# Performance work log

Hardware: AMD Instinct MI355X
Metric: run time of the kernel (lower is better)

## Reference

```python
import jax, jax.numpy as jnp
import numpy as np

EMBED_DIM = 1024
NUM_HEADS = 16
HEAD_DIM = EMBED_DIM // NUM_HEADS
SCALE = HEAD_DIM ** -0.5


def setup_inputs() -> dict:
    key = jax.random.key(0)
    ks = jax.random.split(key, 9)
    B, S, D = 32, 577, EMBED_DIM
    std = 1.0 / np.sqrt(D)
    inp = {
        "hidden_states": jax.random.normal(ks[0], (B, S, D), dtype=jnp.float32),
        "q_w": jax.random.normal(ks[1], (D, D), dtype=jnp.float32) * std,
        "q_b": jax.random.normal(ks[2], (D,), dtype=jnp.float32) * 0.01,
        "k_w": jax.random.normal(ks[3], (D, D), dtype=jnp.float32) * std,
        "k_b": jax.random.normal(ks[4], (D,), dtype=jnp.float32) * 0.01,
        "v_w": jax.random.normal(ks[5], (D, D), dtype=jnp.float32) * std,
        "v_b": jax.random.normal(ks[6], (D,), dtype=jnp.float32) * 0.01,
        "o_w": jax.random.normal(ks[7], (D, D), dtype=jnp.float32) * std,
        "o_b": jax.random.normal(ks[8], (D,), dtype=jnp.float32) * 0.01,
    }
    return inp


def reference(hidden_states, q_w, q_b, k_w, k_b, v_w, v_b, o_w, o_b):
    B, S, D = hidden_states.shape
    H, Dh = NUM_HEADS, HEAD_DIM

    def proj(w, b):
        # torch Linear: x @ w.T + b ; reshape to [B, H, S, Dh]
        y = jnp.einsum('bsd,ed->bse', hidden_states, w) + b
        return y.reshape(B, S, H, Dh).transpose(0, 2, 1, 3)

    q = proj(q_w, q_b)
    k = proj(k_w, k_b)
    v = proj(v_w, v_b)

    scores = jnp.einsum('bhqd,bhkd->bhqk', q * SCALE, k)  # [B,H,S,S]
    attn = jax.nn.softmax(scores, axis=-1)
    out = jnp.einsum('bhqk,bhkd->bhqd', attn, v)  # [B,H,S,Dh]
    out = out.transpose(0, 2, 1, 3).reshape(B, S, D)
    return jnp.einsum('bsd,ed->bse', out, o_w) + o_b
```

## Files before the change

### kernel.cpp

```cpp
#include <hip/hip_runtime.h>
#include <hip/hip_bf16.h>
#include <stdint.h>

#define B_   32
#define S_   577
#define SP   640
#define D_   1024
#define H_   16
#define DH   64
#define BH_  (B_*H_)
#define M_   (B_*S_)
#define MP2  18688
#define SCALE_ 0.125f
#define LOG2E_ 1.44269504088896f

typedef __bf16 bf16;
typedef __bf16 bf16x8 __attribute__((ext_vector_type(8)));
typedef __bf16 bf16x4 __attribute__((ext_vector_type(4)));
typedef float  f32x4  __attribute__((ext_vector_type(4)));

__device__ __forceinline__ void gload16(const bf16* g, bf16* l) {
    __builtin_amdgcn_global_load_lds((__attribute__((address_space(1))) void*)g,
                                     (__attribute__((address_space(3))) void*)l, 16, 0, 0);
}

__global__ void cast_kernel(const float* __restrict__ in, bf16* __restrict__ out, int n4) {
    int i = blockIdx.x * blockDim.x + threadIdx.x;
    if (i >= n4) return;
    float4 v = ((const float4*)in)[i];
    bf16x4 o;
    o[0] = (bf16)v.x; o[1] = (bf16)v.y; o[2] = (bf16)v.z; o[3] = (bf16)v.w;
    ((bf16x4*)out)[i] = o;
}

__global__ void cast4_kernel(const float* __restrict__ w0, const float* __restrict__ w1,
                             const float* __restrict__ w2, const float* __restrict__ w3,
                             bf16* __restrict__ o0, bf16* __restrict__ o1,
                             bf16* __restrict__ o2, bf16* __restrict__ o3) {
    int i = blockIdx.x * blockDim.x + threadIdx.x;
    int seg = i >> 18, r = i & 262143;
    const float* in = (seg == 0) ? w0 : (seg == 1) ? w1 : (seg == 2) ? w2 : w3;
    bf16* out       = (seg == 0) ? o0 : (seg == 1) ? o1 : (seg == 2) ? o2 : o3;
    float4 v = ((const float4*)in)[r];
    bf16x4 o;
    o[0] = (bf16)v.x; o[1] = (bf16)v.y; o[2] = (bf16)v.z; o[3] = (bf16)v.w;
    ((bf16x4*)out)[r] = o;
}

__device__ __forceinline__ void stage256(const bf16* __restrict__ A, const bf16* __restrict__ B,
                                         int m0, int n0, int K, int kt, bf16* SMbuf) {
    const int tid = threadIdx.x;
    const int wave = tid >> 6;
    #pragma unroll
    for (int ld = 0; ld < 8; ++ld) {
        int li  = ld * 512 + tid;
        int row = (li >> 3) & 255;
        int ch  = (li & 7) ^ (row & 7);
        const bf16* g = ((ld < 4) ? (A + (size_t)(m0 + row) * K)
                                  : (B + (size_t)(n0 + row) * K)) + kt * 64 + ch * 8;
        bf16* l = SMbuf + (size_t)(ld * 512 + wave * 64) * 8;
        gload16(g, l);
    }
}

__device__ __forceinline__ void compute256(const bf16* SMbuf, f32x4 acc[8][4],
                                           int wm, int wn, int r16, int c4) {
    #pragma unroll
    for (int kk = 0; kk < 2; ++kk) {
        bf16x8 bq[4];
        #pragma unroll
        for (int j = 0; j < 4; ++j) {
            int row = wn * 64 + j * 16 + r16;
            int c   = (kk * 4 + c4) ^ (row & 7);
            bq[j] = *(const bf16x8*)(SMbuf + 16384 + row * 64 + c * 8);
        }
        #pragma unroll
        for (int i = 0; i < 8; ++i) {
            int row = wm * 128 + i * 16 + r16;
            int c   = (kk * 4 + c4) ^ (row & 7);
            bf16x8 a = *(const bf16x8*)(SMbuf + row * 64 + c * 8);
            #pragma unroll
            for (int j = 0; j < 4; ++j)
                acc[i][j] = __builtin_amdgcn_mfma_f32_16x16x32_bf16(a, bq[j], acc[i][j], 0, 0, 0);
        }
    }
}

__global__ __launch_bounds__(512, 2) void gemm_qkv(const bf16* __restrict__ A, const bf16* __restrict__ Bw,
                                                   const float* __restrict__ qb, const float* __restrict__ kb,
                                                   const float* __restrict__ vb,
                                                   bf16* __restrict__ qk, bf16* __restrict__ vT) {
    __shared__ __align__(16) bf16 SM[2 * 32768];
    const int bx = blockIdx.x;
    const int bm = bx / 12, bn = bx % 12;
    const int m0 = bm * 256, n0 = bn * 256;
    const int tid = threadIdx.x;
    const int lane = tid & 63, wave = tid >> 6;
    const int wm = wave >> 2, wn = wave & 3;
    const int r16 = lane & 15, c4 = lane >> 4;

    f32x4 acc[8][4];
    #pragma unroll
    for (int i = 0; i < 8; ++i)
        #pragma unroll
        for (int j = 0; j < 4; ++j)
            #pragma unroll
            for (int r = 0; r < 4; ++r) acc[i][j][r] = 0.0f;

    stage256(A, Bw, m0, n0, 1024, 0, SM);
    __syncthreads();
    for (int kt = 0; kt < 16; ++kt) {
        if (kt < 15) stage256(A, Bw, m0, n0, 1024, kt + 1, SM + ((kt + 1) & 1) * 32768);
        compute256(SM + (kt & 1) * 32768, acc, wm, wn, r16, c4);
        __syncthreads();
    }

    if (bn < 8) {
        const float* barr = (bn < 4) ? qb : kb;
        const float mul = (bn < 4) ? SCALE_ * LOG2E_ : 1.0f;
        #pragma unroll
        for (int j = 0; j < 4; ++j) {
            int n = n0 + wn * 64 + j * 16 + r16;
            float bias = barr[n & 1023];
            #pragma unroll
            for (int i = 0; i < 8; ++i) {
                #pragma unroll
                for (int r = 0; r < 4; ++r) {
                    int m = m0 + wm * 128 + i * 16 + c4 * 4 + r;
                    if (m < M_) qk[(size_t)m * 2048 + n] = (bf16)((acc[i][j][r] + bias) * mul);
                }
            }
        }
    } else {
        const int bnp = bn - 8;
        bf16* Ts = SM;
        #pragma unroll
        for (int mh = 0; mh < 2; ++mh) {
            if (wm == mh) {
                #pragma unroll
                for (int j = 0; j < 4; ++j) {
                    int nl = wn * 64 + j * 16 + r16;
                    float bias = vb[bnp * 256 + nl];
                    #pragma unroll
                    for (int i = 0; i < 8; ++i) {
                        #pragma unroll
                        for (int r = 0; r < 4; ++r) {
                            int tr = i * 16 + c4 * 4 + r;
                            Ts[tr * 259 + nl] = (bf16)(acc[i][j][r] + bias);
                        }
                    }
                }
            }
            __syncthreads();
            {
                int ml = tid & 127, nh = tid >> 7;
                int gm = m0 + mh * 128 + ml;
                if (gm < M_) {
                    unsigned bb = (unsigned)gm / 577u, s = (unsigned)gm - bb * 577u;
                    bf16* dst = vT + ((size_t)((bb * 16 + bnp * 4 + nh) * 64)) * SP + s;
                    const bf16* src = Ts + ml * 259 + nh * 64;
                    #pragma unroll 8
                    for (int j = 0; j < 64; ++j) dst[(size_t)j * SP] = src[j];
                }
            }
            __syncthreads();
        }
    }
}

__global__ __launch_bounds__(512, 2) void gemm_out(const bf16* __restrict__ A, const bf16* __restrict__ Bw,
                                                   const float* __restrict__ ob, float* __restrict__ out) {
    __shared__ __align__(16) bf16 SM[2 * 32768];
    const int bx = blockIdx.x;
    const int bm = bx >> 2, bn = bx & 3;
    const int m0 = bm * 256, n0 = bn * 256;
    const int tid = threadIdx.x;
    const int lane = tid & 63, wave = tid >> 6;
    const int wm = wave >> 2, wn = wave & 3;
    const int r16 = lane & 15, c4 = lane >> 4;

    f32x4 acc[8][4];
    #pragma unroll
    for (int i = 0; i < 8; ++i)
        #pragma unroll
        for (int j = 0; j < 4; ++j)
            #pragma unroll
            for (int r = 0; r < 4; ++r) acc[i][j][r] = 0.0f;

    stage256(A, Bw, m0, n0, 1024, 0, SM);
    __syncthreads();
    for (int kt = 0; kt < 16; ++kt) {
        if (kt < 15) stage256(A, Bw, m0, n0, 1024, kt + 1, SM + ((kt + 1) & 1) * 32768);
        compute256(SM + (kt & 1) * 32768, acc, wm, wn, r16, c4);
        __syncthreads();
    }

    #pragma unroll
    for (int j = 0; j < 4; ++j) {
        int n = n0 + wn * 64 + j * 16 + r16;
        float bias = ob[n];
        #pragma unroll
        for (int i = 0; i < 8; ++i) {
            #pragma unroll
            for (int r = 0; r < 4; ++r) {
                int m = m0 + wm * 128 + i * 16 + c4 * 4 + r;
                if (m < M_) out[(size_t)m * 1024 + n] = acc[i][j][r] + bias;
            }
        }
    }
}

__global__ __launch_bounds__(256) void attn_kernel(const bf16* __restrict__ qk,
                                                   const bf16* __restrict__ vT, bf16* __restrict__ obuf) {
    __shared__ __align__(16) bf16 KV[2][2][4096];
    __shared__ __align__(16) char Pls[4 * 2 * 2048];
    const int orig = blockIdx.x;
    const int xcd = orig & 7;
    const int t   = orig >> 3;
    const int qt  = t % 5, bhg = t / 5;
    const int bh  = bhg * 8 + xcd;
    const int b   = bh >> 4, h = bh & 15;
    const int tid = threadIdx.x;
    const int lane = tid & 63, wave = tid >> 6;
    const int r16 = lane & 15, c4 = lane >> 4;
    const int q0  = qt * 128 + wave * 32;
    const int swz = (r16 & 7) << 4;

    const bf16* qp = qk + (size_t)(b * 577) * 2048 + h * 64;
    const bf16* kp = qp + 1024;
    const bf16* vp = vT + (size_t)bh * 64 * SP;

    bf16x8 aq[2][2];
    #pragma unroll
    for (int qf = 0; qf < 2; ++qf)
        #pragma unroll
        for (int c = 0; c < 2; ++c)
            aq[qf][c] = *(const bf16x8*)(qp + (size_t)(q0 + qf * 16 + r16) * 2048 + c * 32 + c4 * 8);

    float mi[2] = {-3.0e38f, -3.0e38f};
    float li[2] = {0.0f, 0.0f};
    f32x4 accO[2][4];
    #pragma unroll
    for (int qf = 0; qf < 2; ++qf)
        #pragma unroll
        for (int nt = 0; nt < 4; ++nt)
            #pragma unroll
            for (int r = 0; r < 4; ++r) accO[qf][nt][r] = 0.0f;

    char* pbase = Pls + wave * 4096 + r16 * 128;

    auto stageKV = [&](int kt, int buf) {
        #pragma unroll
        for (int half = 0; half < 2; ++half) {
            int li  = half * 256 + tid;
            int row = li >> 3;
            int ch  = (li & 7) ^ (row & 7);
            bf16* lk = &KV[buf][0][(size_t)(half * 256 + wave * 64) * 8];
            bf16* lv = &KV[buf][1][(size_t)(half * 256 + wave * 64) * 8];
            gload16(kp + (size_t)(kt * 64 + row) * 2048 + ch * 8, lk);
            gload16(vp + (size_t)row * SP + kt * 64 + ch * 8, lv);
        }
    };

    stageKV(0, 0);
    __syncthreads();

    for (int kt = 0; kt < 10; ++kt) {
        const int buf = kt & 1;
        if (kt < 9) stageKV(kt + 1, buf ^ 1);

        bf16x8 kf[4][2];
        #pragma unroll
        for (int nt = 0; nt < 4; ++nt)
            #pragma unroll
            for (int c = 0; c < 2; ++c) {
                int row = nt * 16 + r16;
                int cc  = (c * 4 + c4) ^ (row & 7);
                kf[nt][c] = *(const bf16x8*)(&KV[buf][0][row * 64 + cc * 8]);
            }
        f32x4 sc[2][4];
        #pragma unroll
        for (int qf = 0; qf < 2; ++qf)
            #pragma unroll
            for (int nt = 0; nt < 4; ++nt) {
                f32x4 z = {0.0f, 0.0f, 0.0f, 0.0f};
                z = __builtin_amdgcn_mfma_f32_16x16x32_bf16(kf[nt][0], aq[qf][0], z, 0, 0, 0);
                sc[qf][nt] = __builtin_amdgcn_mfma_f32_16x16x32_bf16(kf[nt][1], aq[qf][1], z, 0, 0, 0);
            }

        #pragma unroll
        for (int qf = 0; qf < 2; ++qf) {
            if (kt == 9) {
                #pragma unroll
                for (int nt = 0; nt < 4; ++nt)
                    #pragma unroll
                    for (int r = 0; r < 4; ++r)
                        if (576 + nt * 16 + c4 * 4 + r >= S_) sc[qf][nt][r] = -3.0e38f;
            }
            float pmax = sc[qf][0][0];
            #pragma unroll
            for (int nt = 0; nt < 4; ++nt)
                #pragma unroll
                for (int r = 0; r < 4; ++r) pmax = fmaxf(pmax, sc[qf][nt][r]);
            pmax = fmaxf(pmax, __shfl_xor(pmax, 16));
            pmax = fmaxf(pmax, __shfl_xor(pmax, 32));

            const bool vrow = (q0 + qf * 16 + r16) < S_;
            int ok = (!vrow) || (pmax <= mi[qf] + 8.0f);
            if (!__all(ok)) {
                float mnew = fmaxf(mi[qf], pmax);
                float fsc  = __builtin_amdgcn_exp2f(mi[qf] - mnew);
                mi[qf] = mnew;
                li[qf] *= fsc;
                float fs0 = __shfl(fsc, c4 * 4 + 0);
                float fs1 = __shfl(fsc, c4 * 4 + 1);
                float fs2 = __shfl(fsc, c4 * 4 + 2);
                float fs3 = __shfl(fsc, c4 * 4 + 3);
                #pragma unroll
                for (int nt = 0; nt < 4; ++nt) {
                    accO[qf][nt][0] *= fs0; accO[qf][nt][1] *= fs1;
                    accO[qf][nt][2] *= fs2; accO[qf][nt][3] *= fs3;
                }
            }
            float p[4][4];
            float rs = 0.0f;
            #pragma unroll
            for (int nt = 0; nt < 4; ++nt)
                #pragma unroll
                for (int r = 0; r < 4; ++r) {
                    p[nt][r] = __builtin_amdgcn_exp2f(sc[qf][nt][r] - mi[qf]);
                    rs += p[nt][r];
                }
            rs += __shfl_xor(rs, 16);
            rs += __shfl_xor(rs, 32);
            li[qf] += rs;
            #pragma unroll
            for (int nt = 0; nt < 4; ++nt) {
                bf16x4 pk;
                pk[0] = (bf16)p[nt][0]; pk[1] = (bf16)p[nt][1];
                pk[2] = (bf16)p[nt][2]; pk[3] = (bf16)p[nt][3];
                *(bf16x4*)(pbase + qf * 2048 + ((nt * 32 + c4 * 8) ^ swz)) = pk;
            }
        }

        bf16x8 vf[4][2];
        #pragma unroll
        for (int ntd = 0; ntd < 4; ++ntd)
            #pragma unroll
            for (int kk = 0; kk < 2; ++kk) {
                int row = ntd * 16 + r16;
                int cc  = (kk * 4 + c4) ^ (row & 7);
                vf[ntd][kk] = *(const bf16x8*)(&KV[buf][1][row * 64 + cc * 8]);
            }
        #pragma unroll
        for (int qf = 0; qf < 2; ++qf) {
            bf16x8 pf[2];
            #pragma unroll
            for (int kk = 0; kk < 2; ++kk)
                pf[kk] = *(const bf16x8*)(pbase + qf * 2048 + ((kk * 64 + c4 * 16) ^ swz));
            #pragma unroll
            for (int ntd = 0; ntd < 4; ++ntd)
                #pragma unroll
                for (int kk = 0; kk < 2; ++kk)
                    accO[qf][ntd] = __builtin_amdgcn_mfma_f32_16x16x32_bf16(pf[kk], vf[ntd][kk], accO[qf][ntd], 0, 0, 0);
        }

        __syncthreads();
    }

    #pragma unroll
    for (int qf = 0; qf < 2; ++qf) {
        float inv = 1.0f / li[qf];
        float rl0 = __shfl(inv, c4 * 4 + 0);
        float rl1 = __shfl(inv, c4 * 4 + 1);
        float rl2 = __shfl(inv, c4 * 4 + 2);
        float rl3 = __shfl(inv, c4 * 4 + 3);
        #pragma unroll
        for (int ntd = 0; ntd < 4; ++ntd) {
            #pragma unroll
            for (int r = 0; r < 4; ++r) {
                int s = q0 + qf * 16 + c4 * 4 + r;
                if (s < S_) {
                    float rl = (r == 0) ? rl0 : (r == 1) ? rl1 : (r == 2) ? rl2 : rl3;
                    obuf[((size_t)(b * S_ + s)) * 1024 + h * 64 + ntd * 16 + r16] =
                        (bf16)(accO[qf][ntd][r] * rl);
                }
            }
        }
    }
}

extern "C" void kernel_launch(void* const* d_in, const int* in_sizes, int n_in,
                              void* d_out, int out_size, void* d_ws, size_t ws_size,
                              hipStream_t stream) {
    const float* hs = (const float*)d_in[0];
    const float* qw = (const float*)d_in[1];
    const float* qb = (const float*)d_in[2];
    const float* kw = (const float*)d_in[3];
    const float* kb = (const float*)d_in[4];
    const float* vw = (const float*)d_in[5];
    const float* vb = (const float*)d_in[6];
    const float* ow = (const float*)d_in[7];
    const float* ob = (const float*)d_in[8];

    char* ws = (char*)d_ws;
    size_t off = 0;
    auto alloc = [&](size_t bytes) { void* p = ws + off; off += (bytes + 255) & ~255UL; return p; };
    bf16* hsA  = (bf16*)alloc((size_t)MP2 * 1024 * 2);
    bf16* wqkv = (bf16*)alloc((size_t)3072 * 1024 * 2);
    bf16* wo   = (bf16*)alloc((size_t)1024 * 1024 * 2);
    bf16* qk   = (bf16*)alloc((size_t)MP2 * 2048 * 2);
    bf16* vT   = (bf16*)alloc((size_t)BH_ * 64 * SP * 2);

    hipMemsetAsync(vT, 0, (size_t)BH_ * 64 * SP * 2, stream);

    int n4h = M_ * 1024 / 4;
    cast_kernel<<<(n4h + 255) / 256, 256, 0, stream>>>(hs, hsA, n4h);
    cast4_kernel<<<4096, 256, 0, stream>>>(qw, kw, vw, ow,
                                           wqkv, wqkv + 1048576, wqkv + 2097152, wo);

    gemm_qkv<<<73 * 12, 512, 0, stream>>>(hsA, wqkv, qb, kb, vb, qk, vT);
    attn_kernel<<<2560, 256, 0, stream>>>(qk, vT, hsA);
    gemm_out<<<73 * 4, 512, 0, stream>>>(hsA, wo, ob, (float*)d_out);
}
```

Before: 370.8 us.

## Halve GEMM K-tile, repack two rows per LDS line, raise occupancy target

Both projection GEMMs now stage K-slices of 32 instead of 64. Two matrix rows are packed per 64-element LDS line under a new XOR swizzle, so each double buffer is half as large and the main loop runs twice as many iterations. Launch bounds are raised to 4 blocks per CU to increase occupancy and overlap. The trade-off is more barriers per tile and much tighter register limits against a 128-float accumulator, which risks spilling.

After: 1.209 ms. +226.0%, slower.

```diff
diff --git a/kernel.cpp b/kernel.cpp
--- a/kernel.cpp
+++ b/kernel.cpp
@@ -52,45 +52,59 @@
     const int tid = threadIdx.x;
     const int wave = tid >> 6;
     #pragma unroll
-    for (int ld = 0; ld < 8; ++ld) {
-        int li  = ld * 512 + tid;
-        int row = (li >> 3) & 255;
-        int ch  = (li & 7) ^ (row & 7);
-        const bf16* g = ((ld < 4) ? (A + (size_t)(m0 + row) * K)
-                                  : (B + (size_t)(n0 + row) * K)) + kt * 64 + ch * 8;
-        bf16* l = SMbuf + (size_t)(ld * 512 + wave * 64) * 8;
+    for (int ld = 0; ld < 4; ++ld) {
+        int ci  = (ld & 1) * 512 + tid;
+        int lr  = ci >> 3;
+        int ch  = (ci & 7) ^ (lr & 7);
+        int row = lr * 2 + (ch >> 2);
+        int kof = (ch & 3) * 8;
+        const bf16* g = ((ld < 2) ? (A + (size_t)(m0 + row) * K)
+                                  : (B + (size_t)(n0 + row) * K)) + kt * 32 + kof;
+        bf16* l = SMbuf + (ld < 2 ? 0 : 8192) + (size_t)((ld & 1) * 512 + wave * 64) * 8;
         gload16(g, l);
     }
 }
 
 __device__ __forceinline__ void compute256(const bf16* SMbuf, f32x4 acc[8][4],
                                            int wm, int wn, int r16, int c4) {
-    #pragma unroll
-    for (int kk = 0; kk < 2; ++kk) {
-        bf16x8 bq[4];
-        #pragma unroll
-        for (int j = 0; j < 4; ++j) {
-            int row = wn * 64 + j * 16 + r16;
-            int c   = (kk * 4 + c4) ^ (row & 7);
-            bq[j] = *(const bf16x8*)(SMbuf + 16384 + row * 64 + c * 8);
-        }
-        #pragma unroll
-        for (int i = 0; i < 8; ++i) {
-            int row = wm * 128 + i * 16 + r16;
-            int c   = (kk * 4 + c4) ^ (row & 7);
-            bf16x8 a = *(const bf16x8*)(SMbuf + row * 64 + c * 8);
-            #pragma unroll
-            for (int j = 0; j < 4; ++j)
-                acc[i][j] = __builtin_amdgcn_mfma_f32_16x16x32_bf16(a, bq[j], acc[i][j], 0, 0, 0);
-        }
-    }
-}
-
-__global__ __launch_bounds__(512, 2) void gemm_qkv(const bf16* __restrict__ A, const bf16* __restrict__ Bw,
+    bf16x8 bq[4];
+    #pragma unroll
+    for (int j = 0; j < 4; ++j) {
+        int row = wn * 64 + j * 16 + r16;
+        int lr  = row >> 1;
+        int cc  = (((row & 1) << 2) + c4) ^ (lr & 7);
+        bq[j] = *(const bf16x8*)(SMbuf + 8192 + lr * 64 + cc * 8);
+    }
+    #pragma unroll
+    for (int i = 0; i < 8; ++i) {
+        int row = wm * 128 + i * 16 + r16;
+        int lr  = row >> 1;
+        int cc  = (((row & 1) << 2) + c4) ^ (lr & 7);
+        bf16x8 a = *(const bf16x8*)(SMbuf + lr * 64 + cc * 8);
+        #pragma unroll
+        for (int j = 0; j < 4; ++j)
+            acc[i][j] = __builtin_amdgcn_mfma_f32_16x16x32_bf16(a, bq[j], acc[i][j], 0, 0, 0);
+    }
+}
+
+__device__ __forceinline__ void gemm_mainloop(const bf16* __restrict__ A, const bf16* __restrict__ Bw,
+                                              int m0, int n0, bf16* SM, f32x4 acc[8][4],
+                                              int wm, int wn, int r16, int c4) {
+    stage256(A, Bw, m0, n0, 1024, 0, SM);
+    __syncthreads();
+    for (int kt = 0; kt < 32; ++kt) {
+        if (kt < 31) stage256(A, Bw, m0, n0, 1024, kt + 1, SM + ((kt + 1) & 1) * 16384);
+        compute256(SM + (kt & 1) * 16384, acc, wm, wn, r16, c4);
+        __syncthreads();
+    }
+}
+
+__global__ __launch_bounds__(512, 4) void gemm_qkv(const bf16* __restrict__ A, const bf16* __restrict__ Bw,
                                                    const float* __restrict__ qb, const float* __restrict__ kb,
                                                    const float* __restrict__ vb,
                                                    bf16* __restrict__ qk, bf16* __restrict__ vT) {
-    __shared__ __align__(16) bf16 SM[2 * 32768];
+    __shared__ __align__(16) char SMc[66304];
+    bf16* SM = (bf16*)SMc;
     const int bx = blockIdx.x;
     const int bm = bx / 12, bn = bx % 12;
     const int m0 = bm * 256, n0 = bn * 256;
@@ -107,13 +121,7 @@
             #pragma unroll
             for (int r = 0; r < 4; ++r) acc[i][j][r] = 0.0f;
 
-    stage256(A, Bw, m0, n0, 1024, 0, SM);
-    __syncthreads();
-    for (int kt = 0; kt < 16; ++kt) {
-        if (kt < 15) stage256(A, Bw, m0, n0, 1024, kt + 1, SM + ((kt + 1) & 1) * 32768);
-        compute256(SM + (kt & 1) * 32768, acc, wm, wn, r16, c4);
-        __syncthreads();
-    }
+    gemm_mainloop(A, Bw, m0, n0, SM, acc, wm, wn, r16, c4);
 
     if (bn < 8) {
         const float* barr = (bn < 4) ? qb : kb;
@@ -133,7 +141,7 @@
         }
     } else {
         const int bnp = bn - 8;
-        bf16* Ts = SM;
+        bf16* Ts = (bf16*)SMc;
         #pragma unroll
         for (int mh = 0; mh < 2; ++mh) {
             if (wm == mh) {
@@ -168,9 +176,9 @@
     }
 }
 
-__global__ __launch_bounds__(512, 2) void gemm_out(const bf16* __restrict__ A, const bf16* __restrict__ Bw,
+__global__ __launch_bounds__(512, 4) void gemm_out(const bf16* __restrict__ A, const bf16* __restrict__ Bw,
                                                    const float* __restrict__ ob, float* __restrict__ out) {
-    __shared__ __align__(16) bf16 SM[2 * 32768];
+    __shared__ __align__(16) bf16 SM[2 * 16384];
     const int bx = blockIdx.x;
     const int bm = bx >> 2, bn = bx & 3;
     const int m0 = bm * 256, n0 = bn * 256;
@@ -187,13 +195,7 @@
             #pragma unroll
             for (int r = 0; r < 4; ++r) acc[i][j][r] = 0.0f;
 
-    stage256(A, Bw, m0, n0, 1024, 0, SM);
-    __syncthreads();
-    for (int kt = 0; kt < 16; ++kt) {
-        if (kt < 15) stage256(A, Bw, m0, n0, 1024, kt + 1, SM + ((kt + 1) & 1) * 32768);
-        compute256(SM + (kt & 1) * 32768, acc, wm, wn, r16, c4);
-        __syncthreads();
-    }
+    gemm_mainloop(A, Bw, m0, n0, SM, acc, wm, wn, r16, c4);
 
     #pragma unroll
     for (int j = 0; j < 4; ++j) {
```

## Halve output GEMM M-tile and reuse single P buffer per wave in attention

Applied to the files above, without the earlier changes.

The output projection GEMM now uses 128x256 tiles with its own staging routine and inline MFMA loop, and launches 580 blocks instead of 292. The aim is to cut the tail-wave imbalance across CUs and halve accumulator register pressure, at the cost of less B-tile reuse per block. In the attention kernel, V fragments are now loaded right after the QK MFMAs. The P scratch buffer is shrunk to one 16-row tile per wave, reused for each query fragment, with the PV MFMAs done right after each softmax. This halves the P shared-memory footprint, which may raise occupancy, but it serialises the two query fragments through the same buffer.

Measured after the change: 369.2 us. About the same (-0.4%).

```diff
diff --git a/kernel.cpp b/kernel.cpp
--- a/kernel.cpp
+++ b/kernel.cpp
@@ -168,30 +168,71 @@
     }
 }
 
+__device__ __forceinline__ void stage_out(const bf16* __restrict__ A, const bf16* __restrict__ B,
+                                          int m0, int n0, int kt, bf16* SMbuf) {
+    const int tid = threadIdx.x;
+    const int wave = tid >> 6;
+    #pragma unroll
+    for (int ld = 0; ld < 2; ++ld) {
+        int li  = ld * 512 + tid;
+        int row = li >> 3;
+        int ch  = (li & 7) ^ (row & 7);
+        gload16(A + (size_t)(m0 + row) * 1024 + kt * 64 + ch * 8,
+                SMbuf + (size_t)(ld * 512 + wave * 64) * 8);
+    }
+    #pragma unroll
+    for (int ld = 0; ld < 4; ++ld) {
+        int li  = ld * 512 + tid;
+        int row = li >> 3;
+        int ch  = (li & 7) ^ (row & 7);
+        gload16(B + (size_t)(n0 + row) * 1024 + kt * 64 + ch * 8,
+                SMbuf + 8192 + (size_t)(ld * 512 + wave * 64) * 8);
+    }
+}
+
 __global__ __launch_bounds__(512, 2) void gemm_out(const bf16* __restrict__ A, const bf16* __restrict__ Bw,
                                                    const float* __restrict__ ob, float* __restrict__ out) {
-    __shared__ __align__(16) bf16 SM[2 * 32768];
+    __shared__ __align__(16) bf16 SM[2 * 24576];
     const int bx = blockIdx.x;
     const int bm = bx >> 2, bn = bx & 3;
-    const int m0 = bm * 256, n0 = bn * 256;
+    const int m0 = bm * 128, n0 = bn * 256;
     const int tid = threadIdx.x;
     const int lane = tid & 63, wave = tid >> 6;
     const int wm = wave >> 2, wn = wave & 3;
     const int r16 = lane & 15, c4 = lane >> 4;
 
-    f32x4 acc[8][4];
-    #pragma unroll
-    for (int i = 0; i < 8; ++i)
+    f32x4 acc[4][4];
+    #pragma unroll
+    for (int i = 0; i < 4; ++i)
         #pragma unroll
         for (int j = 0; j < 4; ++j)
             #pragma unroll
             for (int r = 0; r < 4; ++r) acc[i][j][r] = 0.0f;
 
-    stage256(A, Bw, m0, n0, 1024, 0, SM);
+    stage_out(A, Bw, m0, n0, 0, SM);
     __syncthreads();
     for (int kt = 0; kt < 16; ++kt) {
-        if (kt < 15) stage256(A, Bw, m0, n0, 1024, kt + 1, SM + ((kt + 1) & 1) * 32768);
-        compute256(SM + (kt & 1) * 32768, acc, wm, wn, r16, c4);
+        if (kt < 15) stage_out(A, Bw, m0, n0, kt + 1, SM + ((kt + 1) & 1) * 24576);
+        const bf16* SMbuf = SM + (kt & 1) * 24576;
+        #pragma unroll
+        for (int kk = 0; kk < 2; ++kk) {
+            bf16x8 bq[4];
+            #pragma unroll
+            for (int j = 0; j < 4; ++j) {
+                int row = wn * 64 + j * 16 + r16;
+                int c   = (kk * 4 + c4) ^ (row & 7);
+                bq[j] = *(const bf16x8*)(SMbuf + 8192 + row * 64 + c * 8);
+            }
+            #pragma unroll
+            for (int i = 0; i < 4; ++i) {
+                int row = wm * 64 + i * 16 + r16;
+                int c   = (kk * 4 + c4) ^ (row & 7);
+                bf16x8 a = *(const bf16x8*)(SMbuf + row * 64 + c * 8);
+                #pragma unroll
+                for (int j = 0; j < 4; ++j)
+                    acc[i][j] = __builtin_amdgcn_mfma_f32_16x16x32_bf16(a, bq[j], acc[i][j], 0, 0, 0);
+            }
+        }
         __syncthreads();
     }
 
@@ -200,10 +241,10 @@
         int n = n0 + wn * 64 + j * 16 + r16;
         float bias = ob[n];
         #pragma unroll
-        for (int i = 0; i < 8; ++i) {
+        for (int i = 0; i < 4; ++i) {
             #pragma unroll
             for (int r = 0; r < 4; ++r) {
-                int m = m0 + wm * 128 + i * 16 + c4 * 4 + r;
+                int m = m0 + wm * 64 + i * 16 + c4 * 4 + r;
                 if (m < M_) out[(size_t)m * 1024 + n] = acc[i][j][r] + bias;
             }
         }
@@ -213,7 +254,7 @@
 __global__ __launch_bounds__(256) void attn_kernel(const bf16* __restrict__ qk,
                                                    const bf16* __restrict__ vT, bf16* __restrict__ obuf) {
     __shared__ __align__(16) bf16 KV[2][2][4096];
-    __shared__ __align__(16) char Pls[4 * 2 * 2048];
+    __shared__ __align__(16) char Pls[4 * 2048];
     const int orig = blockIdx.x;
     const int xcd = orig & 7;
     const int t   = orig >> 3;
@@ -247,7 +288,7 @@
             #pragma unroll
             for (int r = 0; r < 4; ++r) accO[qf][nt][r] = 0.0f;
 
-    char* pbase = Pls + wave * 4096 + r16 * 128;
+    char* pbase = Pls + wave * 2048 + r16 * 128;
 
     auto stageKV = [&](int kt, int buf) {
         #pragma unroll
@@ -286,6 +327,16 @@
                 f32x4 z = {0.0f, 0.0f, 0.0f, 0.0f};
                 z = __builtin_amdgcn_mfma_f32_16x16x32_bf16(kf[nt][0], aq[qf][0], z, 0, 0, 0);
                 sc[qf][nt] = __builtin_amdgcn_mfma_f32_16x16x32_bf16(kf[nt][1], aq[qf][1], z, 0, 0, 0);
+            }
+
+        bf16x8 vf[4][2];
+        #pragma unroll
+        for (int ntd = 0; ntd < 4; ++ntd)
+            #pragma unroll
+            for (int kk = 0; kk < 2; ++kk) {
+                int row = ntd * 16 + r16;
+                int cc  = (kk * 4 + c4) ^ (row & 7);
+                vf[ntd][kk] = *(const bf16x8*)(&KV[buf][1][row * 64 + cc * 8]);
             }
 
         #pragma unroll
@@ -339,25 +390,13 @@
                 bf16x4 pk;
                 pk[0] = (bf16)p[nt][0]; pk[1] = (bf16)p[nt][1];
                 pk[2] = (bf16)p[nt][2]; pk[3] = (bf16)p[nt][3];
-                *(bf16x4*)(pbase + qf * 2048 + ((nt * 32 + c4 * 8) ^ swz)) = pk;
-            }
-        }
-
-        bf16x8 vf[4][2];
-        #pragma unroll
-        for (int ntd = 0; ntd < 4; ++ntd)
-            #pragma unroll
-            for (int kk = 0; kk < 2; ++kk) {
-                int row = ntd * 16 + r16;
-                int cc  = (kk * 4 + c4) ^ (row & 7);
-                vf[ntd][kk] = *(const bf16x8*)(&KV[buf][1][row * 64 + cc * 8]);
-            }
-        #pragma unroll
-        for (int qf = 0; qf < 2; ++qf) {
+                *(bf16x4*)(pbase + ((nt * 32 + c4 * 8) ^ swz)) = pk;
+            }
+
             bf16x8 pf[2];
             #pragma unroll
             for (int kk = 0; kk < 2; ++kk)
-                pf[kk] = *(const bf16x8*)(pbase + qf * 2048 + ((kk * 64 + c4 * 16) ^ swz));
+                pf[kk] = *(const bf16x8*)(pbase + ((kk * 64 + c4 * 16) ^ swz));
             #pragma unroll
             for (int ntd = 0; ntd < 4; ++ntd)
                 #pragma unroll
@@ -421,5 +460,5 @@
 
     gemm_qkv<<<73 * 12, 512, 0, stream>>>(hsA, wqkv, qb, kb, vb, qk, vT);
     attn_kernel<<<2560, 256, 0, stream>>>(qk, vT, hsA);
-    gemm_out<<<73 * 4, 512, 0, stream>>>(hsA, wo, ob, (float*)d_out);
-}
+    gemm_out<<<145 * 4, 512, 0, stream>>>(hsA, wo, ob, (float*)d_out);
+}
```
